# Performance work log

Measured on AMD Instinct MI355X. Metric: run time of the kernel, lower is better.

## Reference

```python
import jax, jax.numpy as jnp
import numpy as np

B, S, D, H = 2, 2048, 1024, 16
HD = D // H  # head_dim = 64


def setup_inputs() -> dict:
    key = jax.random.key(0)
    ks = jax.random.split(key, 6)
    scale = 0.02
    x = jax.random.normal(ks[0], (B, S, D), dtype=jnp.float32)
    Wq = jax.random.normal(ks[1], (D, D), dtype=jnp.float32) * scale
    Wk = jax.random.normal(ks[2], (D, D), dtype=jnp.float32) * scale
    Wv = jax.random.normal(ks[3], (D, D), dtype=jnp.float32) * scale
    Wo = jax.random.normal(ks[4], (D, D), dtype=jnp.float32) * scale
    bo = jnp.zeros((D,), dtype=jnp.float32)
    return {"x": x, "Wq": Wq, "Wk": Wk, "Wv": Wv, "Wo": Wo, "bo": bo}


def reference(x, Wq, Wk, Wv, Wo, bo):
    b, s, _ = x.shape
    # Linear projections (qkv_bias=False), split into heads: [b, h, s, hd]
    def split_heads(t):
        return t.reshape(b, s, H, HD).transpose(0, 2, 1, 3)
    q = split_heads(x @ Wq)
    k = split_heads(x @ Wk)
    v = split_heads(x @ Wv)
    # Scaled dot-product scores: [b, h, s, s]
    scores = jnp.einsum('bhqd,bhkd->bhqk', q, k) / jnp.sqrt(jnp.float32(HD))
    # Causal mask: triu(ones, diagonal=1) positions -> -inf
    causal = jnp.triu(jnp.ones((s, s), dtype=bool), k=1)
    scores = jnp.where(causal, -jnp.inf, scores)
    attn = jax.nn.softmax(scores, axis=-1)
    # dropout p=0.0 (eval-equivalent): identity
    ctx = jnp.einsum('bhqk,bhkd->bhqd', attn, v)  # [b, h, s, hd]
    ctx = ctx.transpose(0, 2, 1, 3).reshape(b, s, D)
    return ctx @ Wo + bo
```

## Files before the change

kernel.cpp:

```cpp
#include <hip/hip_runtime.h>
#include <math.h>

#define BB 2
#define SS 2048
#define DD 1024
#define HH 16
#define HD 64
#define MM (BB * SS)

typedef __bf16 bf16;
typedef __attribute__((ext_vector_type(8))) __bf16 bf16x8;
typedef __attribute__((ext_vector_type(4))) __bf16 bf16x4;
typedef __attribute__((ext_vector_type(4))) float f32x4;

__device__ __forceinline__ void gld_lds16(const void* g, void* l) {
    __builtin_amdgcn_global_load_lds(
        (const __attribute__((address_space(1))) void*)g,
        (__attribute__((address_space(3))) void*)l, 16, 0, 0);
}

__global__ __launch_bounds__(256) void prep(
    const float* __restrict__ x,
    const float* __restrict__ W0, const float* __restrict__ W1,
    const float* __restrict__ W2, const float* __restrict__ W3,
    bf16* __restrict__ xb, bf16* __restrict__ Wt)
{
    __shared__ float tile[32][33];
    const int z = blockIdx.z;
    if (z < 4) {
        const float* W = (z == 0) ? W0 : (z == 1) ? W1 : (z == 2) ? W2 : W3;
        bf16* O = Wt + (size_t)z * DD * DD;
        const int tx = threadIdx.x & 31, ty = threadIdx.x >> 5;
        const int k0 = blockIdx.y * 32, n0 = blockIdx.x * 32;
#pragma unroll
        for (int i = 0; i < 4; ++i)
            tile[ty + i * 8][tx] = W[(size_t)(k0 + ty + i * 8) * DD + n0 + tx];
        __syncthreads();
#pragma unroll
        for (int i = 0; i < 4; ++i)
            O[(size_t)(n0 + ty + i * 8) * DD + k0 + tx] = (bf16)tile[tx][ty + i * 8];
    } else {
        const int lb = (z - 4) * 1024 + blockIdx.y * 32 + blockIdx.x;
        const size_t i = ((size_t)lb * 256 + threadIdx.x) * 8;
        const float4 a = *(const float4*)(x + i);
        const float4 b = *(const float4*)(x + i + 4);
        bf16x8 o;
        o[0] = (bf16)a.x; o[1] = (bf16)a.y; o[2] = (bf16)a.z; o[3] = (bf16)a.w;
        o[4] = (bf16)b.x; o[5] = (bf16)b.y; o[6] = (bf16)b.z; o[7] = (bf16)b.w;
        *(bf16x8*)(xb + i) = o;
    }
}

__device__ __forceinline__ void mfma_core(
    const bf16* __restrict__ A, const bf16* __restrict__ Bt,
    int bm, int bn, int K, bf16* As, bf16* Bs, f32x4 (&acc)[4][4])
{
    const int t = threadIdx.x;
    const int w = t >> 6;
    const int l16 = t & 15, quad = (t >> 4) & 3;
    const int wr = w >> 1, wc = w & 1;
    const int arow = t >> 2;
    const int achk = (t & 3) << 3;

    const bf16* gA = A + (size_t)(bm + arow) * K + achk;
    const bf16* gB = Bt + (size_t)(bn + arow) * K + achk;
    bf16* lA = As + w * 512;
    bf16* lB = Bs + w * 512;

    for (int k0 = 0; k0 < K; k0 += 32) {
        gld_lds16(gA + k0, lA);
        gld_lds16(gA + (size_t)64 * K + k0, lA + 2048);
        gld_lds16(gB + k0, lB);
        gld_lds16(gB + (size_t)64 * K + k0, lB + 2048);
        __syncthreads();

        bf16x8 af[4], bv[4];
#pragma unroll
        for (int i = 0; i < 4; ++i) {
            af[i] = *(const bf16x8*)(As + (wr * 64 + i * 16 + l16) * 32 + quad * 8);
            bv[i] = *(const bf16x8*)(Bs + (wc * 64 + i * 16 + l16) * 32 + quad * 8);
        }
#pragma unroll
        for (int mi = 0; mi < 4; ++mi)
#pragma unroll
            for (int ni = 0; ni < 4; ++ni)
                acc[mi][ni] = __builtin_amdgcn_mfma_f32_16x16x32_bf16(
                    af[mi], bv[ni], acc[mi][ni], 0, 0, 0);
        __syncthreads();
    }
}

__global__ __launch_bounds__(256) void gemm_qkv(
    const bf16* __restrict__ xb, const bf16* __restrict__ Wt,
    bf16* __restrict__ Qb, bf16* __restrict__ Kb, bf16* __restrict__ Vb)
{
    __shared__ __align__(16) bf16 As[128 * 32];
    __shared__ __align__(16) bf16 Bs[128 * 32];
    const int bm = blockIdx.y * 128, bn = blockIdx.x * 128, z = blockIdx.z;

    f32x4 acc[4][4] = {};
    mfma_core(xb, Wt + (size_t)z * DD * DD, bm, bn, DD, As, Bs, acc);

    const int t = threadIdx.x;
    const int w = t >> 6, l16 = t & 15, quad = (t >> 4) & 3;
    const int wr = w >> 1, wc = w & 1;
    bf16* outp = (z == 0) ? Qb : (z == 1) ? Kb : Vb;

#pragma unroll
    for (int mi = 0; mi < 4; ++mi) {
#pragma unroll
        for (int ni = 0; ni < 4; ++ni) {
            const int col = bn + wc * 64 + ni * 16 + l16;
            const int h = col >> 6, hd = col & 63;
#pragma unroll
            for (int r = 0; r < 4; ++r) {
                const int row = bm + wr * 64 + mi * 16 + quad * 4 + r;
                const int b = row >> 11, s = row & (SS - 1);
                size_t addr;
                if (z < 2) addr = ((size_t)((b * HH + h) * SS + s)) * HD + hd;
                else       addr = ((size_t)((b * HH + h) * HD + hd)) * SS + s;
                outp[addr] = (bf16)acc[mi][ni][r];
            }
        }
    }
}

__global__ __launch_bounds__(256) void gemm_out(
    const bf16* __restrict__ ctx, const bf16* __restrict__ Wto,
    const float* __restrict__ bias, float* __restrict__ out)
{
    __shared__ __align__(16) bf16 As[128 * 32];
    __shared__ __align__(16) bf16 Bs[128 * 32];
    const int bm = blockIdx.y * 128, bn = blockIdx.x * 128;

    f32x4 acc[4][4] = {};
    mfma_core(ctx, Wto, bm, bn, DD, As, Bs, acc);

    const int t = threadIdx.x;
    const int w = t >> 6, l16 = t & 15, quad = (t >> 4) & 3;
    const int wr = w >> 1, wc = w & 1;

#pragma unroll
    for (int mi = 0; mi < 4; ++mi) {
#pragma unroll
        for (int ni = 0; ni < 4; ++ni) {
            const int col = bn + wc * 64 + ni * 16 + l16;
            const float b = bias[col];
#pragma unroll
            for (int r = 0; r < 4; ++r) {
                const int row = bm + wr * 64 + mi * 16 + quad * 4 + r;
                out[(size_t)row * DD + col] = acc[mi][ni][r] + b;
            }
        }
    }
}

#define PROWS 72
__global__ __launch_bounds__(256) void attn_flash(
    const bf16* __restrict__ Q, const bf16* __restrict__ K,
    const bf16* __restrict__ Vt, bf16* __restrict__ ctx)
{
    __shared__ __align__(16) bf16 Ks[2][64 * 64];
    __shared__ __align__(16) bf16 Vs[2][64 * 64];
    __shared__ __align__(16) bf16 Pl[4][16 * PROWS];

    const int t = threadIdx.x;
    const int w = t >> 6;
    const int lane = t & 63;
    const int l16 = lane & 15, quad = lane >> 4;

    const int L  = blockIdx.x;
    const int bh = L & 31;
    const int qg = 31 - (L >> 5);
    const int q0b = qg * 64;
    const int q0w = q0b + w * 16;

    const bf16* Qp = Q  + ((size_t)bh * SS + q0w) * HD;
    const bf16* Kp = K  + (size_t)bh * SS * HD;
    const bf16* Vp = Vt + (size_t)bh * HD * SS;
    bf16* Pw = &Pl[w][0];

    const bf16x8 bQ0 = *(const bf16x8*)(Qp + l16 * HD + quad * 8);
    const bf16x8 bQ1 = *(const bf16x8*)(Qp + l16 * HD + 32 + quad * 8);

    f32x4 accO[4] = {{0,0,0,0},{0,0,0,0},{0,0,0,0},{0,0,0,0}};
    float Lr = 0.f;
    const float cl2 = 0.125f * 1.44269504f;
    const int qrow = q0w + l16;

    const int r8 = lane >> 3, cs = lane & 7;
    const int nkt = qg + 1;

#pragma unroll
    for (int j = 0; j < 2; ++j) {
        const int region = w * 2 + j;
        const int row = region * 8 + r8;
        const int c = (cs - row) & 7;
        gld_lds16(Kp + (size_t)row * HD + c * 8, &Ks[0][region * 512]);
        gld_lds16(Vp + (size_t)row * SS + c * 8, &Vs[0][region * 512]);
    }

    for (int kt = 0; kt < nkt; ++kt) {
        const int kb = kt * 64;
        const int buf = kt & 1;
        __syncthreads();

        if (kt + 1 < nkt) {
            const int kb2 = kb + 64;
#pragma unroll
            for (int j = 0; j < 2; ++j) {
                const int region = w * 2 + j;
                const int row = region * 8 + r8;
                const int c = (cs - row) & 7;
                gld_lds16(Kp + (size_t)(kb2 + row) * HD + c * 8, &Ks[buf ^ 1][region * 512]);
                gld_lds16(Vp + (size_t)row * SS + kb2 + c * 8, &Vs[buf ^ 1][region * 512]);
            }
        }

        const bf16* Kbuf = &Ks[buf][0];
        const bf16* Vbuf = &Vs[buf][0];

        f32x4 St[4] = {{0,0,0,0},{0,0,0,0},{0,0,0,0},{0,0,0,0}};
#pragma unroll
        for (int mi = 0; mi < 4; ++mi) {
            const int row = mi * 16 + l16;
            const bf16x8 a0 = *(const bf16x8*)(Kbuf + row * 64 + ((quad + row) & 7) * 8);
            const bf16x8 a1 = *(const bf16x8*)(Kbuf + row * 64 + ((quad + 4 + row) & 7) * 8);
            St[mi] = __builtin_amdgcn_mfma_f32_16x16x32_bf16(a0, bQ0, St[mi], 0, 0, 0);
            St[mi] = __builtin_amdgcn_mfma_f32_16x16x32_bf16(a1, bQ1, St[mi], 0, 0, 0);
        }

        if (kb + 63 > q0w) {
#pragma unroll
            for (int mi = 0; mi < 4; ++mi)
#pragma unroll
                for (int r = 0; r < 4; ++r)
                    if (kb + mi * 16 + quad * 4 + r > qrow) St[mi][r] = -1e30f;
        }

        float rs = 0.f;
#pragma unroll
        for (int mi = 0; mi < 4; ++mi) {
            bf16x4 pk;
#pragma unroll
            for (int r = 0; r < 4; ++r) {
                const float p = exp2f(St[mi][r] * cl2);
                rs += p;
                pk[r] = (bf16)p;
            }
            *(bf16x4*)(Pw + l16 * PROWS + mi * 16 + quad * 4) = pk;
        }
        rs += __shfl_xor(rs, 16);
        rs += __shfl_xor(rs, 32);
        Lr += rs;

#pragma unroll
        for (int kc = 0; kc < 2; ++kc) {
            const bf16x8 bP = *(const bf16x8*)(Pw + l16 * PROWS + kc * 32 + quad * 8);
#pragma unroll
            for (int mi = 0; mi < 4; ++mi) {
                const int row = mi * 16 + l16;
                const bf16x8 aV = *(const bf16x8*)(
                    Vbuf + row * 64 + (((kc * 4 + quad) + row) & 7) * 8);
                accO[mi] = __builtin_amdgcn_mfma_f32_16x16x32_bf16(aV, bP, accO[mi], 0, 0, 0);
            }
        }
    }

    const float rinv = 1.0f / Lr;
    const int b = bh >> 4, h = bh & (HH - 1);
    bf16* op = ctx + ((size_t)(b * SS + q0w + l16)) * DD + h * HD;
#pragma unroll
    for (int mi = 0; mi < 4; ++mi) {
        bf16x4 o;
#pragma unroll
        for (int r = 0; r < 4; ++r) o[r] = (bf16)(accO[mi][r] * rinv);
        *(bf16x4*)(op + mi * 16 + quad * 4) = o;
    }
}

extern "C" void kernel_launch(void* const* d_in, const int* in_sizes, int n_in,
                              void* d_out, int out_size, void* d_ws, size_t ws_size,
                              hipStream_t stream)
{
    const float* x  = (const float*)d_in[0];
    const float* Wq = (const float*)d_in[1];
    const float* Wk = (const float*)d_in[2];
    const float* Wv = (const float*)d_in[3];
    const float* Wo = (const float*)d_in[4];
    const float* bo = (const float*)d_in[5];
    float* out = (float*)d_out;

    const size_t chunk = (size_t)MM * DD;
    bf16* xb  = (bf16*)d_ws;
    bf16* Wt  = xb + chunk;
    bf16* Qb  = Wt + 4 * (size_t)DD * DD;
    bf16* Kb  = Qb + chunk;
    bf16* Vb  = Kb + chunk;
    bf16* ctx = Vb + chunk;

    prep<<<dim3(32, 32, 6), dim3(256), 0, stream>>>(x, Wq, Wk, Wv, Wo, xb, Wt);

    gemm_qkv<<<dim3(DD / 128, MM / 128, 3), dim3(256), 0, stream>>>(xb, Wt, Qb, Kb, Vb);

    attn_flash<<<dim3(BB * HH * (SS / 64)), dim3(256), 0, stream>>>(Qb, Kb, Vb, ctx);

    gemm_out<<<dim3(DD / 128, MM / 128), dim3(256), 0, stream>>>(
        ctx, Wt + 3 * (size_t)DD * DD, bo, out);
}
```

Measured before the change: 189.3 us.

## Keep softmax probabilities in registers and fold scale into Q projection

The P matrix is no longer round-tripped through LDS. Instead the exp'd scores feed 16x16x16 MFMAs directly as register operands, with the V reads swizzled to match the accumulator layout. The softmax scale times log2(e) is folded into the Q projection epilogue, so the inner loop uses a raw exp2 builtin without a multiply. The KV loop is unrolled by two with static buffer indices, the query tiles are reordered to balance causal work across blocks, and launch bounds request 4 blocks per CU. The cost is twice as many smaller MFMAs for PV, and the epilogue applies the scale to Q before the bf16 rounding.

```diff
diff --git a/kernel.cpp b/kernel.cpp
--- a/kernel.cpp
+++ b/kernel.cpp
@@ -11,7 +11,19 @@
 typedef __bf16 bf16;
 typedef __attribute__((ext_vector_type(8))) __bf16 bf16x8;
 typedef __attribute__((ext_vector_type(4))) __bf16 bf16x4;
+typedef __attribute__((ext_vector_type(4))) short short4v;
 typedef __attribute__((ext_vector_type(4))) float f32x4;
+
+#if __has_builtin(__builtin_amdgcn_exp2f)
+#define EXP2F(x) __builtin_amdgcn_exp2f(x)
+#else
+#define EXP2F(x) exp2f(x)
+#endif
+
+__device__ __forceinline__ f32x4 pv_mfma16(bf16x4 a, short4v b, f32x4 c) {
+    return __builtin_amdgcn_mfma_f32_16x16x16bf16_1k(
+        __builtin_bit_cast(short4v, a), b, c, 0, 0, 0);
+}
 
 __device__ __forceinline__ void gld_lds16(const void* g, void* l) {
     __builtin_amdgcn_global_load_lds(
@@ -105,6 +117,7 @@
     const int w = t >> 6, l16 = t & 15, quad = (t >> 4) & 3;
     const int wr = w >> 1, wc = w & 1;
     bf16* outp = (z == 0) ? Qb : (z == 1) ? Kb : Vb;
+    const float scl = (z == 0) ? 0.18033688011f : 1.0f;
 
 #pragma unroll
     for (int mi = 0; mi < 4; ++mi) {
@@ -119,7 +132,7 @@
                 size_t addr;
                 if (z < 2) addr = ((size_t)((b * HH + h) * SS + s)) * HD + hd;
                 else       addr = ((size_t)((b * HH + h) * HD + hd)) * SS + s;
-                outp[addr] = (bf16)acc[mi][ni][r];
+                outp[addr] = (bf16)(acc[mi][ni][r] * scl);
             }
         }
     }
@@ -155,14 +168,12 @@
     }
 }
 
-#define PROWS 72
-__global__ __launch_bounds__(256) void attn_flash(
+__global__ __launch_bounds__(256, 4) void attn_flash(
     const bf16* __restrict__ Q, const bf16* __restrict__ K,
     const bf16* __restrict__ Vt, bf16* __restrict__ ctx)
 {
     __shared__ __align__(16) bf16 Ks[2][64 * 64];
     __shared__ __align__(16) bf16 Vs[2][64 * 64];
-    __shared__ __align__(16) bf16 Pl[4][16 * PROWS];
 
     const int t = threadIdx.x;
     const int w = t >> 6;
@@ -171,111 +182,130 @@
 
     const int L  = blockIdx.x;
     const int bh = L & 31;
-    const int qg = 31 - (L >> 5);
+    const int idx = L >> 5;
+    const int pg = idx >> 3, pr = idx & 7;
+    const int qg = (pg == 0) ? 31 - pr : (pg == 1) ? pr
+                 : (pg == 2) ? 23 - pr : 8 + pr;
     const int q0b = qg * 64;
     const int q0w = q0b + w * 16;
+    const int qrow = q0w + l16;
+    const int nkt = qg + 1;
 
     const bf16* Qp = Q  + ((size_t)bh * SS + q0w) * HD;
     const bf16* Kp = K  + (size_t)bh * SS * HD;
     const bf16* Vp = Vt + (size_t)bh * HD * SS;
-    bf16* Pw = &Pl[w][0];
 
     const bf16x8 bQ0 = *(const bf16x8*)(Qp + l16 * HD + quad * 8);
     const bf16x8 bQ1 = *(const bf16x8*)(Qp + l16 * HD + 32 + quad * 8);
 
+    const int r8 = lane >> 3, cs = lane & 7;
+    const int rowA = (w * 2) * 8 + r8, rowB = (w * 2 + 1) * 8 + r8;
+    const int cA = (cs - rowA) & 7, cB = (cs - rowB) & 7;
+    const bf16* gK0 = Kp + (size_t)rowA * HD + cA * 8;
+    const bf16* gK1 = Kp + (size_t)rowB * HD + cB * 8;
+    const bf16* gV0 = Vp + (size_t)rowA * SS + cA * 8;
+    const bf16* gV1 = Vp + (size_t)rowB * SS + cB * 8;
+    bf16* const lK0 = &Ks[0][(w * 2) * 512];
+    bf16* const lK1 = &Ks[0][(w * 2 + 1) * 512];
+    bf16* const lV0 = &Vs[0][(w * 2) * 512];
+    bf16* const lV1 = &Vs[0][(w * 2 + 1) * 512];
+
+#define STAGE(BUF, KB) do {                                              \
+        gld_lds16(gK0 + (size_t)(KB) * HD, lK0 + (BUF) * 4096);          \
+        gld_lds16(gK1 + (size_t)(KB) * HD, lK1 + (BUF) * 4096);          \
+        gld_lds16(gV0 + (KB),              lV0 + (BUF) * 4096);          \
+        gld_lds16(gV1 + (KB),              lV1 + (BUF) * 4096);          \
+    } while (0)
+
+    const int offK0 = l16 * 64 + ((quad + l16) & 7) * 8;
+    const int offK1 = l16 * 64 + ((quad + 4 + l16) & 7) * 8;
+    int offV[4];
+#pragma unroll
+    for (int mi = 0; mi < 4; ++mi)
+        offV[mi] = l16 * 64 + ((((quad >> 1) + 2 * mi + l16) & 7) * 8)
+                 + (quad & 1) * 4;
+
+    const bf16* const KsB = &Ks[0][0];
+    const bf16* const VsB = &Vs[0][0];
+
     f32x4 accO[4] = {{0,0,0,0},{0,0,0,0},{0,0,0,0},{0,0,0,0}};
     float Lr = 0.f;
-    const float cl2 = 0.125f * 1.44269504f;
-    const int qrow = q0w + l16;
-
-    const int r8 = lane >> 3, cs = lane & 7;
-    const int nkt = qg + 1;
-
-#pragma unroll
-    for (int j = 0; j < 2; ++j) {
-        const int region = w * 2 + j;
-        const int row = region * 8 + r8;
-        const int c = (cs - row) & 7;
-        gld_lds16(Kp + (size_t)row * HD + c * 8, &Ks[0][region * 512]);
-        gld_lds16(Vp + (size_t)row * SS + c * 8, &Vs[0][region * 512]);
-    }
-
-    for (int kt = 0; kt < nkt; ++kt) {
-        const int kb = kt * 64;
-        const int buf = kt & 1;
-        __syncthreads();
-
-        if (kt + 1 < nkt) {
-            const int kb2 = kb + 64;
-#pragma unroll
-            for (int j = 0; j < 2; ++j) {
-                const int region = w * 2 + j;
-                const int row = region * 8 + r8;
-                const int c = (cs - row) & 7;
-                gld_lds16(Kp + (size_t)(kb2 + row) * HD + c * 8, &Ks[buf ^ 1][region * 512]);
-                gld_lds16(Vp + (size_t)row * SS + kb2 + c * 8, &Vs[buf ^ 1][region * 512]);
-            }
-        }
-
-        const bf16* Kbuf = &Ks[buf][0];
-        const bf16* Vbuf = &Vs[buf][0];
-
-        f32x4 St[4] = {{0,0,0,0},{0,0,0,0},{0,0,0,0},{0,0,0,0}};
-#pragma unroll
-        for (int mi = 0; mi < 4; ++mi) {
-            const int row = mi * 16 + l16;
-            const bf16x8 a0 = *(const bf16x8*)(Kbuf + row * 64 + ((quad + row) & 7) * 8);
-            const bf16x8 a1 = *(const bf16x8*)(Kbuf + row * 64 + ((quad + 4 + row) & 7) * 8);
-            St[mi] = __builtin_amdgcn_mfma_f32_16x16x32_bf16(a0, bQ0, St[mi], 0, 0, 0);
-            St[mi] = __builtin_amdgcn_mfma_f32_16x16x32_bf16(a1, bQ1, St[mi], 0, 0, 0);
-        }
-
-        if (kb + 63 > q0w) {
-#pragma unroll
-            for (int mi = 0; mi < 4; ++mi)
-#pragma unroll
-                for (int r = 0; r < 4; ++r)
-                    if (kb + mi * 16 + quad * 4 + r > qrow) St[mi][r] = -1e30f;
-        }
-
-        float rs = 0.f;
-#pragma unroll
-        for (int mi = 0; mi < 4; ++mi) {
-            bf16x4 pk;
-#pragma unroll
-            for (int r = 0; r < 4; ++r) {
-                const float p = exp2f(St[mi][r] * cl2);
-                rs += p;
-                pk[r] = (bf16)p;
-            }
-            *(bf16x4*)(Pw + l16 * PROWS + mi * 16 + quad * 4) = pk;
-        }
-        rs += __shfl_xor(rs, 16);
-        rs += __shfl_xor(rs, 32);
-        Lr += rs;
-
-#pragma unroll
-        for (int kc = 0; kc < 2; ++kc) {
-            const bf16x8 bP = *(const bf16x8*)(Pw + l16 * PROWS + kc * 32 + quad * 8);
-#pragma unroll
-            for (int mi = 0; mi < 4; ++mi) {
-                const int row = mi * 16 + l16;
-                const bf16x8 aV = *(const bf16x8*)(
-                    Vbuf + row * 64 + (((kc * 4 + quad) + row) & 7) * 8);
-                accO[mi] = __builtin_amdgcn_mfma_f32_16x16x32_bf16(aV, bP, accO[mi], 0, 0, 0);
-            }
-        }
-    }
+
+#define TILE(BUF, KB) do {                                                   \
+        f32x4 St[4] = {{0,0,0,0},{0,0,0,0},{0,0,0,0},{0,0,0,0}};             \
+        _Pragma("unroll")                                                    \
+        for (int mi = 0; mi < 4; ++mi) {                                     \
+            const bf16x8 a0 = *(const bf16x8*)(KsB + (BUF) * 4096            \
+                                               + mi * 1024 + offK0);         \
+            const bf16x8 a1 = *(const bf16x8*)(KsB + (BUF) * 4096            \
+                                               + mi * 1024 + offK1);         \
+            St[mi] = __builtin_amdgcn_mfma_f32_16x16x32_bf16(                \
+                a0, bQ0, St[mi], 0, 0, 0);                                   \
+            St[mi] = __builtin_amdgcn_mfma_f32_16x16x32_bf16(                \
+                a1, bQ1, St[mi], 0, 0, 0);                                   \
+        }                                                                    \
+        if ((KB) + 63 > q0w) {                                               \
+            _Pragma("unroll")                                                \
+            for (int mi = 0; mi < 4; ++mi)                                   \
+                _Pragma("unroll")                                            \
+                for (int rr = 0; rr < 4; ++rr)                               \
+                    if ((KB) + mi * 16 + quad * 4 + rr > qrow)               \
+                        St[mi][rr] = -1e30f;                                 \
+        }                                                                    \
+        float rs = 0.f;                                                      \
+        short4v pb[4];                                                       \
+        _Pragma("unroll")                                                    \
+        for (int mi = 0; mi < 4; ++mi) {                                     \
+            bf16x4 pk;                                                       \
+            _Pragma("unroll")                                                \
+            for (int rr = 0; rr < 4; ++rr) {                                 \
+                const float p = EXP2F(St[mi][rr]);                           \
+                rs += p;                                                     \
+                pk[rr] = (bf16)p;                                            \
+            }                                                                \
+            pb[mi] = __builtin_bit_cast(short4v, pk);                        \
+        }                                                                    \
+        rs += __shfl_xor(rs, 16);                                            \
+        rs += __shfl_xor(rs, 32);                                            \
+        Lr += rs;                                                            \
+        _Pragma("unroll")                                                    \
+        for (int mi = 0; mi < 4; ++mi) {                                     \
+            _Pragma("unroll")                                                \
+            for (int db = 0; db < 4; ++db) {                                 \
+                const bf16x4 aV = *(const bf16x4*)(VsB + (BUF) * 4096        \
+                                                   + db * 1024 + offV[mi]);  \
+                accO[db] = pv_mfma16(aV, pb[mi], accO[db]);                  \
+            }                                                                \
+        }                                                                    \
+    } while (0)
+
+    STAGE(0, 0);
+    int kb = 0;
+    for (int kt = 0; kt + 2 <= nkt; kt += 2) {
+        __syncthreads();
+        STAGE(1, kb + 64);
+        TILE(0, kb);
+        __syncthreads();
+        if (kt + 2 < nkt) STAGE(0, kb + 128);
+        TILE(1, kb + 64);
+        kb += 128;
+    }
+    if (nkt & 1) {
+        __syncthreads();
+        TILE(0, kb);
+    }
+#undef TILE
+#undef STAGE
 
     const float rinv = 1.0f / Lr;
     const int b = bh >> 4, h = bh & (HH - 1);
     bf16* op = ctx + ((size_t)(b * SS + q0w + l16)) * DD + h * HD;
 #pragma unroll
-    for (int mi = 0; mi < 4; ++mi) {
+    for (int db = 0; db < 4; ++db) {
         bf16x4 o;
 #pragma unroll
-        for (int r = 0; r < 4; ++r) o[r] = (bf16)(accO[mi][r] * rinv);
-        *(bf16x4*)(op + mi * 16 + quad * 4) = o;
+        for (int rr = 0; rr < 4; ++rr) o[rr] = (bf16)(accO[db][rr] * rinv);
+        *(bf16x4*)(op + db * 16 + quad * 4) = o;
     }
 }
 
```

Result: no change. 187.2 us (-1.1%).
